# Optimization experiments

Measured on AMD Instinct MI355X. Metric: run time of the kernel, lower is better.

The kernel has to match this reference:

```python
import jax, jax.numpy as jnp
import numpy as np

# ---- constants from OtLlamaAttention __init__ defaults / chosen config ----
Q_LEVELS = 256
Q_LUT_MIN = 0.02004
SMOOTH = 0.9           # stat_smooth_factor (EMA)
Q_SEED = 0
HEAD_DIM = 128
SCALING = HEAD_DIM ** -0.5
N_HEADS, N_KV_HEADS = 32, 8
GROUPS = N_HEADS // N_KV_HEADS  # num_key_value_groups


def _update_qstats(x, old_mm, sf=SMOOTH):
    # q_min_max_quantiles is None -> plain min/max; EMA once stats are finite.
    cur = jax.lax.stop_gradient(jnp.stack([x.min(), x.max()]).astype(old_mm.dtype))
    return jnp.where(jnp.isfinite(old_mm).all(), sf * old_mm + (1.0 - sf) * cur, cur)


def _repeat_kv(x, n_rep):
    # [B, KVH, S, D] -> [B, KVH*n_rep, S, D]
    return jnp.repeat(x, n_rep, axis=1)


def _fq(x, lo, hi, levels=Q_LEVELS):
    # deterministic uniform fake-quant with straight-through estimator
    scale = (hi - lo) / (levels - 1)
    q = jnp.round((jnp.clip(x, lo, hi) - lo) / scale) * scale + lo
    return x + jax.lax.stop_gradient(q - x)


def _fq_b_lut(b, lo, hi, lut_min, levels=Q_LEVELS):
    # weight-side quantization: uniform levels, magnitudes below the modulator
    # LUT minimum (relative to full scale) are not representable -> 0
    scale = (hi - lo) / (levels - 1)
    q = jnp.round((jnp.clip(b, lo, hi) - lo) / scale) * scale + lo
    full_scale = jnp.maximum(jnp.abs(lo), jnp.abs(hi))
    q = jnp.where(jnp.abs(q) < lut_min * full_scale, 0.0, q)
    return b + jax.lax.stop_gradient(q - b)


def _fq_stoch(x, lo, hi, rkey, levels=Q_LEVELS):
    # seeded stochastic rounding on the (optical) accumulator output
    scale = (hi - lo) / (levels - 1)
    t = (jnp.clip(x, lo, hi) - lo) / scale
    u = jax.lax.stop_gradient(jax.random.uniform(rkey, x.shape, dtype=x.dtype))
    q = jnp.floor(t + u) * scale + lo
    return x + jax.lax.stop_gradient(q - x)


def _quantized_matmul(a, b, a_mm, b_mm, o_mm, rkey, skip_quantize=False):
    if skip_quantize:
        return jnp.matmul(a, b)
    aq = _fq(a, a_mm[0], a_mm[1])
    bq = _fq_b_lut(b, b_mm[0], b_mm[1], Q_LUT_MIN)
    out = jnp.matmul(aq, bq)
    return _fq_stoch(out, o_mm[0], o_mm[1], rkey)


def setup_inputs() -> dict:
    key0 = jax.random.key(0)
    k1, k2, k3 = jax.random.split(key0, 3)
    B, S, D = 1, 2048, HEAD_DIM
    query = jax.random.normal(k1, (B, N_HEADS, S, D), dtype=jnp.float32)
    key = jax.random.normal(k2, (B, N_KV_HEADS, S, D), dtype=jnp.float32)
    value = jax.random.normal(k3, (B, N_KV_HEADS, S, D), dtype=jnp.float32)
    causal = jnp.tril(jnp.ones((S, S), dtype=bool))
    attention_mask = jnp.where(causal, 0.0, -1e9).astype(jnp.float32)[None, None]
    inf = jnp.float32(jnp.inf)
    fresh = jnp.array([inf, -inf], dtype=jnp.float32)
    return {
        "query": query, "key": key, "value": value,
        "attention_mask": attention_mask,
        "query_min_max": fresh, "key_min_max": fresh, "qk_min_max": fresh,
        "attn_min_max": jnp.array([0.0, 1.0], dtype=jnp.float32),
        "value_min_max": fresh, "av_min_max": fresh,
    }


def reference(query, key, value, attention_mask, query_min_max, key_min_max,
              qk_min_max, attn_min_max, value_min_max, av_min_max):
    rk = jax.random.key(Q_SEED)
    rk_qk, rk_av = jax.random.split(rk)

    # ---- no_grad stat updates (used immediately, as torch copies in-place) ----
    q_mm = _update_qstats(query, query_min_max)
    k_mm = _update_qstats(key, key_min_max)

    key_states = _repeat_kv(key, GROUPS)      # [B,H,S,D]
    value_states = _repeat_kv(value, GROUPS)

    # qk_min_max starts non-finite -> seeded from an unquantized pass
    raw_qk = jax.lax.stop_gradient(
        jnp.einsum("bhqd,bhkd->bhqk", query, key_states) * SCALING)
    qk_mm = _update_qstats(raw_qk, qk_min_max)

    # ---- quantized QK^T ----
    attn_weights = _quantized_matmul(
        query, jnp.swapaxes(key_states, -1, -2), q_mm, k_mm, qk_mm, rk_qk)
    attn_weights = attn_weights * SCALING
    attn_weights = attn_weights + attention_mask[:, :, :, : key_states.shape[-2]]
    attn_weights = jax.nn.softmax(attn_weights.astype(jnp.float32), axis=-1
                                  ).astype(query.dtype)
    # dropout p=0.0 -> identity

    a_mm = _update_qstats(attn_weights, attn_min_max)
    v_mm = _update_qstats(value_states, value_min_max)
    raw_av = jax.lax.stop_gradient(jnp.matmul(attn_weights, value_states))
    av_mm = _update_qstats(raw_av, av_min_max)

    # ---- quantized AV ----
    attn_output = _quantized_matmul(
        attn_weights, value_states, a_mm, v_mm, av_mm, rk_av,
        skip_quantize=False)

    attn_output = jnp.swapaxes(attn_output, 1, 2)  # [B,S,H,D]
    return attn_output, attn_weights


if __name__ == "__main__":
    out = reference(**setup_inputs())
    print(out[0].shape, out[1].shape)
```

## Files before the change

kernel.cpp:

```cpp
#include <hip/hip_runtime.h>
#include <stdint.h>
#include <math.h>

#pragma clang fp contract(off)

#define NH 32
#define NKVH 8
#define SEQ 2048
#define HD 128
#define SCALING_F 0.08838834764831845f
#define OUT0_N (SEQ*NH*HD)

typedef __attribute__((ext_vector_type(8))) short bf16x8;
typedef __attribute__((ext_vector_type(8))) _Float16 f16x8;
typedef __attribute__((ext_vector_type(8))) unsigned short u16x8;
typedef __attribute__((ext_vector_type(4))) float f32x4;

__host__ __device__ __forceinline__ void tf2x32(uint32_t k0, uint32_t k1,
    uint32_t x0, uint32_t x1, uint32_t* o0, uint32_t* o1) {
  uint32_t k2 = k0 ^ k1 ^ 0x1BD11BDAu;
  x0 += k0; x1 += k1;
#define TFR(r) { x0 += x1; x1 = (x1 << (r)) | (x1 >> (32 - (r))); x1 ^= x0; }
  TFR(13) TFR(15) TFR(26) TFR(6)
  x0 += k1; x1 += k2 + 1u;
  TFR(17) TFR(29) TFR(16) TFR(24)
  x0 += k2; x1 += k0 + 2u;
  TFR(13) TFR(15) TFR(26) TFR(6)
  x0 += k0; x1 += k1 + 3u;
  TFR(17) TFR(29) TFR(16) TFR(24)
  x0 += k1; x1 += k2 + 4u;
  TFR(13) TFR(15) TFR(26) TFR(6)
  x0 += k2; x1 += k0 + 5u;
#undef TFR
  *o0 = x0; *o1 = x1;
}

__device__ __forceinline__ float tf_uniform(uint32_t k0, uint32_t k1, uint32_t idx) {
  uint32_t a, b;
  tf2x32(k0, k1, 0u, idx, &a, &b);
  uint32_t bits = a ^ b;
  return __uint_as_float((bits >> 9) | 0x3f800000u) - 1.0f;
}

__device__ __forceinline__ unsigned fmono(float x) {
  unsigned u = __float_as_uint(x);
  return (u >> 31) ? ~u : (u | 0x80000000u);
}
__device__ __forceinline__ float funmono(unsigned m) {
  return __uint_as_float((m >> 31) ? (m ^ 0x80000000u) : ~m);
}

__device__ __forceinline__ void push_minmax(unsigned* slots, unsigned cm, unsigned cM) {
  volatile unsigned* vs = (volatile unsigned*)slots;
  if (cm < vs[0]) atomicMin(&slots[0], cm);
  if (cM > vs[1]) atomicMax(&slots[1], cM);
}

__device__ __forceinline__ unsigned short f2bf(float x) {
  return (unsigned short)(__float_as_uint(x) >> 16);
}

__device__ __forceinline__ void f16split(float x, unsigned short* h, unsigned short* l) {
  _Float16 hf = (_Float16)x;
  float r = x - (float)hf;
  _Float16 lf = (_Float16)r;
  *h = __builtin_bit_cast(unsigned short, hf);
  *l = __builtin_bit_cast(unsigned short, lf);
}

__device__ __forceinline__ float fq_st_i(float x, float lo, float hi, float scale,
                                         float scinv, float u) {
  float c = fminf(fmaxf(x, lo), hi);
  float t = (c - lo) * scinv;
  return floorf(t + u) * scale + lo;
}

#define SWZ_OFF(row, c16) ((((row) * 256) + ((c16) * 16)) ^ (((row) & 7) << 4))

__device__ __forceinline__ void stage_panel(const unsigned short* __restrict__ g,
                                            int rowstride, unsigned short* s, int tid) {
#pragma unroll
  for (int it = 0; it < 8; ++it) {
    const int i = it * 256 + tid;
    const int row = i >> 4, c16 = i & 15;
    const u16x8 val = *(const u16x8*)&g[(size_t)row * rowstride + c16 * 8];
    *(u16x8*)((char*)s + SWZ_OFF(row, c16)) = val;
  }
}

__device__ __forceinline__ f16x8 frag_h(const unsigned short* s, int row, int c16) {
  return *(const f16x8*)((const char*)s + SWZ_OFF(row, c16));
}
__device__ __forceinline__ bf16x8 frag_b(const unsigned short* s, int row, int c16) {
  return *(const bf16x8*)((const char*)s + SWZ_OFF(row, c16));
}

__global__ void init_ws(unsigned* su) {
  int t = threadIdx.x;
  if (t < 12) su[t] = (t & 1) ? 0u : 0xFFFFFFFFu;
}

__global__ void finalize_kernel(const unsigned* __restrict__ slots,
                                const float* __restrict__ oldmm,
                                float* __restrict__ outc) {
  if (threadIdx.x == 0) {
    float clo = funmono(slots[0]), chi = funmono(slots[1]);
    float o0 = oldmm[0], o1 = oldmm[1];
    bool fin = isfinite(o0) && isfinite(o1);
    float lo = fin ? (0.9f * o0 + 0.1f * clo) : clo;
    float hi = fin ? (0.9f * o1 + 0.1f * chi) : chi;
    float sc = (hi - lo) / 255.0f;
    outc[0] = lo;
    outc[1] = hi;
    outc[2] = sc;
    outc[3] = 0.02004f * fmaxf(fabsf(lo), fabsf(hi));
    outc[4] = 1.0f / sc;
  }
}

__global__ __launch_bounds__(256) void minmax_kernel(const float4* __restrict__ x,
                                                     int n4, unsigned* __restrict__ slots) {
  float lmin = INFINITY, lmax = -INFINITY;
  for (int i = blockIdx.x * blockDim.x + threadIdx.x; i < n4; i += gridDim.x * blockDim.x) {
    float4 a = x[i];
    lmin = fminf(lmin, fminf(fminf(a.x, a.y), fminf(a.z, a.w)));
    lmax = fmaxf(lmax, fmaxf(fmaxf(a.x, a.y), fmaxf(a.z, a.w)));
  }
  __shared__ unsigned bmin, bmax;
  if (threadIdx.x == 0) { bmin = 0xFFFFFFFFu; bmax = 0u; }
  __syncthreads();
  atomicMin(&bmin, fmono(lmin));
  atomicMax(&bmax, fmono(lmax));
  __syncthreads();
  if (threadIdx.x == 0) push_minmax(slots, bmin, bmax);
}

__global__ __launch_bounds__(256) void quant_q_kernel(const float* __restrict__ q,
    unsigned short* __restrict__ qnb, unsigned short* __restrict__ qh,
    unsigned short* __restrict__ ql, const float* __restrict__ cw) {
  const float lo = cw[0], hi = cw[1], sc = cw[2];
  int idx = blockIdx.x * 256 + threadIdx.x;
  float4 x = ((const float4*)q)[idx];
  float xa[4] = {x.x, x.y, x.z, x.w};
  ushort4 o, oh, ol;
  unsigned short* op = (unsigned short*)&o;
  unsigned short* ohp = (unsigned short*)&oh;
  unsigned short* olp = (unsigned short*)&ol;
#pragma unroll
  for (int j = 0; j < 4; ++j) {
    float n = rintf((fminf(fmaxf(xa[j], lo), hi) - lo) / sc);
    op[j] = f2bf(n);
    f16split(xa[j], &ohp[j], &olp[j]);
  }
  ((ushort4*)qnb)[idx] = o;
  ((ushort4*)qh)[idx] = oh;
  ((ushort4*)ql)[idx] = ol;
}

__global__ __launch_bounds__(256) void quant_k_kernel(const float* __restrict__ k,
    unsigned short* __restrict__ kzb, unsigned short* __restrict__ kmb,
    unsigned short* __restrict__ kh, unsigned short* __restrict__ kl,
    float* __restrict__ Zk, float* __restrict__ Mk, const float* __restrict__ cw) {
  const float lo = cw[8], hi = cw[9], sc = cw[10], thr = cw[11];
  const int tid = threadIdx.x;
  const int row = blockIdx.x * 8 + (tid >> 5);
  const int c4 = (tid & 31) * 4;
  float4 x = *(const float4*)&k[(size_t)row * HD + c4];
  float xa[4] = {x.x, x.y, x.z, x.w};
  ushort4 zo, mo, ho, lo_;
  unsigned short* zp = (unsigned short*)&zo;
  unsigned short* mp = (unsigned short*)&mo;
  unsigned short* hp = (unsigned short*)&ho;
  unsigned short* lp = (unsigned short*)&lo_;
  float zs = 0.f, ms = 0.f;
#pragma unroll
  for (int j = 0; j < 4; ++j) {
    float m = rintf((fminf(fmaxf(xa[j], lo), hi) - lo) / sc);
    float kq = m * sc + lo;
    float z = (fabsf(kq) < thr) ? 0.f : 1.f;
    float mq = z * m;
    zs += z; ms += mq;
    zp[j] = f2bf(z); mp[j] = f2bf(mq);
    f16split(xa[j], &hp[j], &lp[j]);
  }
  *(ushort4*)&kzb[(size_t)row * HD + c4] = zo;
  *(ushort4*)&kmb[(size_t)row * HD + c4] = mo;
  *(ushort4*)&kh[(size_t)row * HD + c4] = ho;
  *(ushort4*)&kl[(size_t)row * HD + c4] = lo_;
#pragma unroll
  for (int off = 16; off > 0; off >>= 1) {
    zs += __shfl_xor(zs, off);
    ms += __shfl_xor(ms, off);
  }
  if ((tid & 31) == 0) { Zk[row] = zs; Mk[row] = ms; }
}

__global__ __launch_bounds__(256) void quant_v_kernel(const float* __restrict__ v,
    unsigned short* __restrict__ vzT, unsigned short* __restrict__ vmT,
    unsigned short* __restrict__ vhT, unsigned short* __restrict__ vlT,
    const float* __restrict__ cw) {
  const float lo = cw[16], hi = cw[17], sc = cw[18], thr = cw[19];
  const int kvh = blockIdx.y, dg = blockIdx.x;
  const int tid = threadIdx.x;
  for (int ch = 0; ch < 8; ++ch) {
    int kp = ch * 256 + tid;
    float4 x = *(const float4*)&v[((size_t)(kvh * SEQ + kp)) * HD + dg * 4];
    float xa[4] = {x.x, x.y, x.z, x.w};
#pragma unroll
    for (int j = 0; j < 4; ++j) {
      float m = rintf((fminf(fmaxf(xa[j], lo), hi) - lo) / sc);
      float vq = m * sc + lo;
      float z = (fabsf(vq) < thr) ? 0.f : 1.f;
      float mq = z * m;
      size_t o = ((size_t)(kvh * HD + dg * 4 + j)) * SEQ + kp;
      vzT[o] = f2bf(z);
      vmT[o] = f2bf(mq);
      unsigned short hb, lb;
      f16split(xa[j], &hb, &lb);
      vhT[o] = hb;
      vlT[o] = lb;
    }
  }
}

__global__ __launch_bounds__(256, 2) void qk_raw_mfma(
    const unsigned short* __restrict__ qh, const unsigned short* __restrict__ ql,
    const unsigned short* __restrict__ kh, const unsigned short* __restrict__ kl,
    unsigned* __restrict__ slots) {
  __shared__ __align__(16) unsigned short s_h[128 * 128];
  __shared__ __align__(16) unsigned short s_l[128 * 128];
  const int kbi = blockIdx.x, qbi = blockIdx.y, h = blockIdx.z;
  const int kvh = h >> 2;
  const int tid = threadIdx.x;
  const int wid = tid >> 6, lane = tid & 63;
  const int fr = lane & 15, fg = lane >> 4;
  const int qrow0 = qbi * 128 + wid * 32;
  const int kcol0 = kbi * 128;
  const unsigned short* qhg = qh + (size_t)h * SEQ * HD;
  const unsigned short* qlg = ql + (size_t)h * SEQ * HD;

  stage_panel(kh + ((size_t)kvh * SEQ + kcol0) * HD, HD, s_h, tid);
  stage_panel(kl + ((size_t)kvh * SEQ + kcol0) * HD, HD, s_l, tid);
  __syncthreads();

  f32x4 acc[2][8];
  const f32x4 z4 = {0.f, 0.f, 0.f, 0.f};
#pragma unroll
  for (int rg = 0; rg < 2; ++rg)
#pragma unroll
    for (int cg = 0; cg < 8; ++cg) acc[rg][cg] = z4;

#pragma unroll
  for (int ks = 0; ks < 4; ++ks) {
    const int d0 = ks * 32 + fg * 8;
    const int c16 = ks * 4 + fg;
    const f16x8 a0h = *(const f16x8*)&qhg[(size_t)(qrow0 + fr) * HD + d0];
    const f16x8 a0l = *(const f16x8*)&qlg[(size_t)(qrow0 + fr) * HD + d0];
    const f16x8 a1h = *(const f16x8*)&qhg[(size_t)(qrow0 + 16 + fr) * HD + d0];
    const f16x8 a1l = *(const f16x8*)&qlg[(size_t)(qrow0 + 16 + fr) * HD + d0];
#pragma unroll
    for (int cg = 0; cg < 8; ++cg) {
      const f16x8 bh = frag_h(s_h, cg * 16 + fr, c16);
      const f16x8 bl = frag_h(s_l, cg * 16 + fr, c16);
      acc[0][cg] = __builtin_amdgcn_mfma_f32_16x16x32_f16(a0h, bh, acc[0][cg], 0, 0, 0);
      acc[0][cg] = __builtin_amdgcn_mfma_f32_16x16x32_f16(a0h, bl, acc[0][cg], 0, 0, 0);
      acc[0][cg] = __builtin_amdgcn_mfma_f32_16x16x32_f16(a0l, bh, acc[0][cg], 0, 0, 0);
      acc[1][cg] = __builtin_amdgcn_mfma_f32_16x16x32_f16(a1h, bh, acc[1][cg], 0, 0, 0);
      acc[1][cg] = __builtin_amdgcn_mfma_f32_16x16x32_f16(a1h, bl, acc[1][cg], 0, 0, 0);
      acc[1][cg] = __builtin_amdgcn_mfma_f32_16x16x32_f16(a1l, bh, acc[1][cg], 0, 0, 0);
    }
  }
  float lmin = INFINITY, lmax = -INFINITY;
#pragma unroll
  for (int rg = 0; rg < 2; ++rg)
#pragma unroll
    for (int cg = 0; cg < 8; ++cg)
#pragma unroll
      for (int r = 0; r < 4; ++r) {
        const float rv = acc[rg][cg][r] * SCALING_F;
        lmin = fminf(lmin, rv);
        lmax = fmaxf(lmax, rv);
      }
  __shared__ unsigned bmin, bmax;
  if (tid == 0) { bmin = 0xFFFFFFFFu; bmax = 0u; }
  __syncthreads();
  atomicMin(&bmin, fmono(lmin));
  atomicMax(&bmax, fmono(lmax));
  __syncthreads();
  if (tid == 0) push_minmax(slots, bmin, bmax);
}

__global__ __launch_bounds__(256, 2) void qk_quant_kernel(
    const unsigned short* __restrict__ qnb, const unsigned short* __restrict__ kzb,
    const unsigned short* __restrict__ kmb, const float* __restrict__ Zk,
    const float* __restrict__ Mk, float* __restrict__ qdot,
    const float* __restrict__ cw) {
  const int kbi = blockIdx.x, qbi = blockIdx.y, h = blockIdx.z;
  if (kbi > qbi) return;
  __shared__ __align__(16) unsigned short s_z[128 * 128];
  __shared__ __align__(16) unsigned short s_m[128 * 128];
  const int kvh = h >> 2;
  const float qlo = cw[0], qsc = cw[2];
  const float klo = cw[8], ksc = cw[10];
  const int tid = threadIdx.x;
  const int wid = tid >> 6, lane = tid & 63;
  const int fr = lane & 15, fg = lane >> 4;
  const int qrow0 = qbi * 128 + wid * 32;
  const int kcol0 = kbi * 128;
  const unsigned short* qg = qnb + (size_t)h * SEQ * HD;

  stage_panel(kzb + ((size_t)kvh * SEQ + kcol0) * HD, HD, s_z, tid);
  stage_panel(kmb + ((size_t)kvh * SEQ + kcol0) * HD, HD, s_m, tid);
  __syncthreads();

  f32x4 P[2][8], R[2][8];
  const f32x4 z4 = {0.f, 0.f, 0.f, 0.f};
#pragma unroll
  for (int rg = 0; rg < 2; ++rg)
#pragma unroll
    for (int cg = 0; cg < 8; ++cg) { P[rg][cg] = z4; R[rg][cg] = z4; }

#pragma unroll
  for (int ks = 0; ks < 4; ++ks) {
    const int d0 = ks * 32 + fg * 8;
    const int c16 = ks * 4 + fg;
    const bf16x8 a0 = *(const bf16x8*)&qg[(size_t)(qrow0 + fr) * HD + d0];
    const bf16x8 a1 = *(const bf16x8*)&qg[(size_t)(qrow0 + 16 + fr) * HD + d0];
#pragma unroll
    for (int cg = 0; cg < 8; ++cg) {
      const bf16x8 bz = frag_b(s_z, cg * 16 + fr, c16);
      const bf16x8 bm = frag_b(s_m, cg * 16 + fr, c16);
      P[0][cg] = __builtin_amdgcn_mfma_f32_16x16x32_bf16(a0, bz, P[0][cg], 0, 0, 0);
      P[1][cg] = __builtin_amdgcn_mfma_f32_16x16x32_bf16(a1, bz, P[1][cg], 0, 0, 0);
      R[0][cg] = __builtin_amdgcn_mfma_f32_16x16x32_bf16(a0, bm, R[0][cg], 0, 0, 0);
      R[1][cg] = __builtin_amdgcn_mfma_f32_16x16x32_bf16(a1, bm, R[1][cg], 0, 0, 0);
    }
  }
#pragma unroll
  for (int cg = 0; cg < 8; ++cg) {
    const int col = kcol0 + cg * 16 + fr;
    const float Z = Zk[kvh * SEQ + col], M = Mk[kvh * SEQ + col];
    const float base = qlo * (klo * Z + ksc * M);
#pragma unroll
    for (int rg = 0; rg < 2; ++rg)
#pragma unroll
      for (int r = 0; r < 4; ++r) {
        const int row = qrow0 + rg * 16 + fg * 4 + r;
        qdot[((size_t)h * SEQ + row) * SEQ + col] =
            base + qsc * (klo * P[rg][cg][r] + ksc * R[rg][cg][r]);
      }
  }
}

__global__ __launch_bounds__(256) void softmax_kernel(
    float* __restrict__ attn, const float* __restrict__ cw,
    unsigned* __restrict__ slots, uint32_t uk0, uint32_t uk1) {
  const int row = blockIdx.x;
  const int qi = row & (SEQ - 1);
  const int tid = threadIdx.x;
  const float lo = cw[24], hi = cw[25], sc = cw[26], sci = cw[28];
  float* prow = attn + (size_t)row * SEQ;
  const uint32_t jbase = (uint32_t)row << 11;

  float vals[8];
  float lmax = -INFINITY;
#pragma unroll
  for (int m = 0; m < 2; ++m) {
    int ki = m * 1024 + tid * 4;
    if (ki <= qi) {
      float4 x4 = *(const float4*)&prow[ki];
      float xa[4] = {x4.x, x4.y, x4.z, x4.w};
#pragma unroll
      for (int j = 0; j < 4; ++j) {
        if (ki + j <= qi) {
          float u = tf_uniform(uk0, uk1, jbase + (uint32_t)(ki + j));
          float lg = fq_st_i(xa[j], lo, hi, sc, sci, u) * SCALING_F;
          vals[m * 4 + j] = lg;
          lmax = fmaxf(lmax, lg);
        } else {
          vals[m * 4 + j] = -INFINITY;
        }
      }
    } else {
      vals[m * 4 + 0] = vals[m * 4 + 1] = vals[m * 4 + 2] = vals[m * 4 + 3] = -INFINITY;
    }
  }

  __shared__ float smax[4], ssum[4], smn[4], smx[4];
#pragma unroll
  for (int off = 32; off > 0; off >>= 1) lmax = fmaxf(lmax, __shfl_xor(lmax, off));
  if ((tid & 63) == 0) smax[tid >> 6] = lmax;
  __syncthreads();
  float rmax = fmaxf(fmaxf(smax[0], smax[1]), fmaxf(smax[2], smax[3]));

  float lsum = 0.f;
#pragma unroll
  for (int e = 0; e < 8; ++e) { vals[e] = __expf(vals[e] - rmax); lsum += vals[e]; }
#pragma unroll
  for (int off = 32; off > 0; off >>= 1) lsum += __shfl_xor(lsum, off);
  if ((tid & 63) == 0) ssum[tid >> 6] = lsum;
  __syncthreads();
  float rinv = 1.0f / (ssum[0] + ssum[1] + ssum[2] + ssum[3]);

  float lmin2 = INFINITY, lmax2 = -INFINITY;
#pragma unroll
  for (int m = 0; m < 2; ++m) {
    int ki = m * 1024 + tid * 4;
    float4 st;
    float* stp = (float*)&st;
#pragma unroll
    for (int j = 0; j < 4; ++j) {
      float w = vals[m * 4 + j] * rinv;
      stp[j] = w;
      lmin2 = fminf(lmin2, w);
      lmax2 = fmaxf(lmax2, w);
    }
    *(float4*)&prow[ki] = st;
  }
#pragma unroll
  for (int off = 32; off > 0; off >>= 1) {
    lmin2 = fminf(lmin2, __shfl_xor(lmin2, off));
    lmax2 = fmaxf(lmax2, __shfl_xor(lmax2, off));
  }
  if ((tid & 63) == 0) { smn[tid >> 6] = lmin2; smx[tid >> 6] = lmax2; }
  __syncthreads();
  if (tid == 0) {
    float mn = fminf(fminf(smn[0], smn[1]), fminf(smn[2], smn[3]));
    float mx = fmaxf(fmaxf(smx[0], smx[1]), fmaxf(smx[2], smx[3]));
    push_minmax(slots, fmono(mn), fmono(mx));
  }
}

__device__ __forceinline__ void pack_split8(const float* __restrict__ p,
                                            f16x8* ah, f16x8* al) {
  float4 w0 = *(const float4*)p;
  float4 w1 = *(const float4*)(p + 4);
  float wa[8] = {w0.x, w0.y, w0.z, w0.w, w1.x, w1.y, w1.z, w1.w};
  f16x8 h, l;
#pragma unroll
  for (int j = 0; j < 8; ++j) {
    _Float16 hf = (_Float16)wa[j];
    h[j] = hf;
    l[j] = (_Float16)(wa[j] - (float)hf);
  }
  *ah = h; *al = l;
}

__global__ __launch_bounds__(256, 2) void av_raw_mfma(
    const float* __restrict__ attn, const unsigned short* __restrict__ vhT,
    const unsigned short* __restrict__ vlT, unsigned* __restrict__ slots) {
  __shared__ __align__(16) unsigned short s_h[128 * 128];
  __shared__ __align__(16) unsigned short s_l[128 * 128];
  const int qbi = (int)gridDim.x - 1 - (int)blockIdx.x;
  const int h = blockIdx.y, kvh = h >> 2;
  const int tid = threadIdx.x;
  const int wid = tid >> 6, lane = tid & 63;
  const int fr = lane & 15, fg = lane >> 4;
  const int qrow0 = qbi * 128 + wid * 32;
  const float* ag = attn + (size_t)h * SEQ * SEQ;
  const unsigned short* bhg = vhT + (size_t)kvh * HD * SEQ;
  const unsigned short* blg = vlT + (size_t)kvh * HD * SEQ;
  const int nc = qbi + 1;
  f32x4 acc[2][8];
  const f32x4 z4 = {0.f, 0.f, 0.f, 0.f};
#pragma unroll
  for (int rg = 0; rg < 2; ++rg)
#pragma unroll
    for (int cg = 0; cg < 8; ++cg) acc[rg][cg] = z4;

  for (int c = 0; c < nc; ++c) {
    __syncthreads();
    stage_panel(bhg + c * 128, SEQ, s_h, tid);
    stage_panel(blg + c * 128, SEQ, s_l, tid);
    __syncthreads();
#pragma unroll
    for (int ks = 0; ks < 4; ++ks) {
      const int kp0 = c * 128 + ks * 32 + fg * 8;
      const int c16 = ks * 4 + fg;
      f16x8 a0h, a0l, a1h, a1l;
      pack_split8(ag + (size_t)(qrow0 + fr) * SEQ + kp0, &a0h, &a0l);
      pack_split8(ag + (size_t)(qrow0 + 16 + fr) * SEQ + kp0, &a1h, &a1l);
#pragma unroll
      for (int cg = 0; cg < 8; ++cg) {
        const f16x8 bh = frag_h(s_h, cg * 16 + fr, c16);
        const f16x8 bl = frag_h(s_l, cg * 16 + fr, c16);
        acc[0][cg] = __builtin_amdgcn_mfma_f32_16x16x32_f16(a0h, bh, acc[0][cg], 0, 0, 0);
        acc[0][cg] = __builtin_amdgcn_mfma_f32_16x16x32_f16(a0h, bl, acc[0][cg], 0, 0, 0);
        acc[0][cg] = __builtin_amdgcn_mfma_f32_16x16x32_f16(a0l, bh, acc[0][cg], 0, 0, 0);
        acc[1][cg] = __builtin_amdgcn_mfma_f32_16x16x32_f16(a1h, bh, acc[1][cg], 0, 0, 0);
        acc[1][cg] = __builtin_amdgcn_mfma_f32_16x16x32_f16(a1h, bl, acc[1][cg], 0, 0, 0);
        acc[1][cg] = __builtin_amdgcn_mfma_f32_16x16x32_f16(a1l, bh, acc[1][cg], 0, 0, 0);
      }
    }
  }
  float lmin = INFINITY, lmax = -INFINITY;
#pragma unroll
  for (int rg = 0; rg < 2; ++rg)
#pragma unroll
    for (int cg = 0; cg < 8; ++cg)
#pragma unroll
      for (int r = 0; r < 4; ++r) {
        lmin = fminf(lmin, acc[rg][cg][r]);
        lmax = fmaxf(lmax, acc[rg][cg][r]);
      }
  __shared__ unsigned bmin, bmax;
  if (tid == 0) { bmin = 0xFFFFFFFFu; bmax = 0u; }
  __syncthreads();
  atomicMin(&bmin, fmono(lmin));
  atomicMax(&bmax, fmono(lmax));
  __syncthreads();
  if (tid == 0) push_minmax(slots, bmin, bmax);
}

__device__ __forceinline__ bf16x8 pack_a8(const float* __restrict__ ar,
                                          float lo, float hi, float sc) {
  float4 w0 = *(const float4*)ar;
  float4 w1 = *(const float4*)(ar + 4);
  float wa[8] = {w0.x, w0.y, w0.z, w0.w, w1.x, w1.y, w1.z, w1.w};
  bf16x8 r;
#pragma unroll
  for (int j = 0; j < 8; ++j) {
    float n = rintf((fminf(fmaxf(wa[j], lo), hi) - lo) / sc);
    r[j] = (short)(__float_as_uint(n) >> 16);
  }
  return r;
}

__global__ __launch_bounds__(256, 2) void av_quant_kernel(
    const float* __restrict__ attn, const unsigned short* __restrict__ vzT,
    const unsigned short* __restrict__ vmT, float* __restrict__ out0,
    const float* __restrict__ cw) {
  __shared__ __align__(16) unsigned short s_z[128 * 128];
  __shared__ __align__(16) unsigned short s_m[128 * 128];
  const int qbi = (int)gridDim.x - 1 - (int)blockIdx.x;
  const int h = blockIdx.y, kvh = h >> 2;
  const float alo = cw[32], ahi = cw[33], asc = cw[34];
  const float vlo = cw[16], vsc = cw[18];
  const int tid = threadIdx.x;
  const int wid = tid >> 6, lane = tid & 63;
  const int fr = lane & 15, fg = lane >> 4;
  const int qrow0 = qbi * 128 + wid * 32;
  const float* ag = attn + (size_t)h * SEQ * SEQ;
  const unsigned short* zg = vzT + (size_t)kvh * HD * SEQ;
  const unsigned short* mg = vmT + (size_t)kvh * HD * SEQ;
  const int nc = qbi + 1;
  f32x4 P[2][8], R[2][8];
  const f32x4 z4 = {0.f, 0.f, 0.f, 0.f};
#pragma unroll
  for (int rg = 0; rg < 2; ++rg)
#pragma unroll
    for (int cg = 0; cg < 8; ++cg) { P[rg][cg] = z4; R[rg][cg] = z4; }

  for (int c = 0; c < nc; ++c) {
    __syncthreads();
    stage_panel(zg + c * 128, SEQ, s_z, tid);
    stage_panel(mg + c * 128, SEQ, s_m, tid);
    __syncthreads();
#pragma unroll
    for (int ks = 0; ks < 4; ++ks) {
      const int kp0 = c * 128 + ks * 32 + fg * 8;
      const int c16 = ks * 4 + fg;
      const bf16x8 a0 = pack_a8(ag + (size_t)(qrow0 + fr) * SEQ + kp0, alo, ahi, asc);
      const bf16x8 a1 = pack_a8(ag + (size_t)(qrow0 + 16 + fr) * SEQ + kp0, alo, ahi, asc);
#pragma unroll
      for (int cg = 0; cg < 8; ++cg) {
        const bf16x8 bz = frag_b(s_z, cg * 16 + fr, c16);
        const bf16x8 bm = frag_b(s_m, cg * 16 + fr, c16);
        P[0][cg] = __builtin_amdgcn_mfma_f32_16x16x32_bf16(a0, bz, P[0][cg], 0, 0, 0);
        P[1][cg] = __builtin_amdgcn_mfma_f32_16x16x32_bf16(a1, bz, P[1][cg], 0, 0, 0);
        R[0][cg] = __builtin_amdgcn_mfma_f32_16x16x32_bf16(a0, bm, R[0][cg], 0, 0, 0);
        R[1][cg] = __builtin_amdgcn_mfma_f32_16x16x32_bf16(a1, bm, R[1][cg], 0, 0, 0);
      }
    }
  }
#pragma unroll
  for (int cg = 0; cg < 8; ++cg) {
    const int dcol = cg * 16 + fr;
#pragma unroll
    for (int rg = 0; rg < 2; ++rg)
#pragma unroll
      for (int r = 0; r < 4; ++r) {
        const int row = qrow0 + rg * 16 + fg * 4 + r;
        out0[((size_t)row * NH + h) * HD + dcol] =
            asc * (vlo * P[rg][cg][r] + vsc * R[rg][cg][r]);
      }
  }
}

__global__ __launch_bounds__(256) void stoch_kernel(float* __restrict__ out0,
                                                    const float* __restrict__ cw,
                                                    uint32_t uk0, uint32_t uk1) {
  int idx = blockIdx.x * 256 + threadIdx.x;
  const float lo = cw[40], hi = cw[41], sc = cw[42], sci = cw[44];
  int qi = idx >> 12;
  int rem = idx & 4095;
  int h = rem >> 7, d = rem & 127;
  uint32_t j = ((uint32_t)h * SEQ + (uint32_t)qi) * HD + (uint32_t)d;
  float x = out0[idx];
  float u = tf_uniform(uk0, uk1, j);
  out0[idx] = fq_st_i(x, lo, hi, sc, sci, u);
}

extern "C" void kernel_launch(void* const* d_in, const int* in_sizes, int n_in,
                              void* d_out, int out_size, void* d_ws, size_t ws_size,
                              hipStream_t stream) {
  (void)in_sizes; (void)n_in; (void)out_size; (void)ws_size;
  const float* q      = (const float*)d_in[0];
  const float* k      = (const float*)d_in[1];
  const float* v      = (const float*)d_in[2];
  const float* q_old  = (const float*)d_in[4];
  const float* k_old  = (const float*)d_in[5];
  const float* qk_old = (const float*)d_in[6];
  const float* a_old  = (const float*)d_in[7];
  const float* v_old  = (const float*)d_in[8];
  const float* av_old = (const float*)d_in[9];
  float* out0 = (float*)d_out;
  float* out1 = out0 + (size_t)OUT0_N;
  unsigned* su = (unsigned*)d_ws;
  float* cw = (float*)d_ws + 16;

  unsigned short* vzT = (unsigned short*)((char*)d_ws + 1024);
  unsigned short* vmT = vzT + (size_t)NKVH * SEQ * HD;
  float* Zk = (float*)(vmT + (size_t)NKVH * SEQ * HD);
  float* Mk = Zk + NKVH * SEQ;

  unsigned short* qnb = (unsigned short*)out0;
  unsigned short* kzb = qnb + (size_t)NH * SEQ * HD;
  unsigned short* kmb = kzb + (size_t)NKVH * SEQ * HD;
  unsigned short* vhT = kmb + (size_t)NKVH * SEQ * HD;
  unsigned short* vlT = vhT + (size_t)NKVH * SEQ * HD;

  unsigned short* qh = (unsigned short*)out1;
  unsigned short* ql = qh + (size_t)NH * SEQ * HD;
  unsigned short* kh = ql + (size_t)NH * SEQ * HD;
  unsigned short* kl = kh + (size_t)NKVH * SEQ * HD;

  uint32_t kq0, kq1, ka0, ka1;
  tf2x32(0u, 0u, 0u, 0u, &kq0, &kq1);
  tf2x32(0u, 0u, 0u, 1u, &ka0, &ka1);

  init_ws<<<1, 32, 0, stream>>>(su);
  minmax_kernel<<<1024, 256, 0, stream>>>((const float4*)q, (NH * SEQ * HD) / 4, su + 0);
  minmax_kernel<<<512, 256, 0, stream>>>((const float4*)k, (NKVH * SEQ * HD) / 4, su + 2);
  minmax_kernel<<<512, 256, 0, stream>>>((const float4*)v, (NKVH * SEQ * HD) / 4, su + 4);
  finalize_kernel<<<1, 1, 0, stream>>>(su + 0, q_old, cw + 0);
  finalize_kernel<<<1, 1, 0, stream>>>(su + 2, k_old, cw + 8);
  finalize_kernel<<<1, 1, 0, stream>>>(su + 4, v_old, cw + 16);

  quant_q_kernel<<<(NH * SEQ * HD) / 4 / 256, 256, 0, stream>>>(q, qnb, qh, ql, cw);
  quant_k_kernel<<<(NKVH * SEQ) / 8, 256, 0, stream>>>(k, kzb, kmb, kh, kl, Zk, Mk, cw);
  quant_v_kernel<<<dim3(32, NKVH), 256, 0, stream>>>(v, vzT, vmT, vhT, vlT, cw);

  qk_raw_mfma<<<dim3(16, 16, NH), 256, 0, stream>>>(qh, ql, kh, kl, su + 6);
  finalize_kernel<<<1, 1, 0, stream>>>(su + 6, qk_old, cw + 24);
  qk_quant_kernel<<<dim3(16, 16, NH), 256, 0, stream>>>(qnb, kzb, kmb, Zk, Mk, out1, cw);

  softmax_kernel<<<NH * SEQ, 256, 0, stream>>>(out1, cw, su + 8, kq0, kq1);
  finalize_kernel<<<1, 1, 0, stream>>>(su + 8, a_old, cw + 32);

  av_raw_mfma<<<dim3(16, NH), 256, 0, stream>>>(out1, vhT, vlT, su + 10);
  finalize_kernel<<<1, 1, 0, stream>>>(su + 10, av_old, cw + 40);
  av_quant_kernel<<<dim3(16, NH), 256, 0, stream>>>(out1, vzT, vmT, out0, cw);

  stoch_kernel<<<OUT0_N / 256, 256, 0, stream>>>(out0, cw, ka0, ka1);
}
```

Baseline: 1.566 ms.

## Fuse raw and quantized AV matmuls; merge minmax, finalize and prep launches

Replaces the separate raw-AV and quantized-AV passes with one fused kernel that reads each attention tile once, packs it into quantized bf16 and f16 hi/lo forms, and runs all MFMA chains together over 64-row query tiles with 64-wide K panels. Moving the V hi/lo buffers into the workspace frees out0 so the fused kernel can write it directly; the fused path runs only when the workspace is at least 18 MB. It also merges the three minmax launches, the three finalize launches and the three quant launches into single kernels to cut launch overhead. The fused kernel keeps more accumulators live (three sets of eight), which raises register pressure, and it uses smaller panels.

```diff
diff --git a/kernel.cpp b/kernel.cpp
--- a/kernel.cpp
+++ b/kernel.cpp
@@ -76,6 +76,7 @@
 }
 
 #define SWZ_OFF(row, c16) ((((row) * 256) + ((c16) * 16)) ^ (((row) & 7) << 4))
+#define SWZ64_OFF(row, c16) ((((row) * 128) + ((c16) * 16)) ^ (((row) & 7) << 4))
 
 __device__ __forceinline__ void stage_panel(const unsigned short* __restrict__ g,
                                             int rowstride, unsigned short* s, int tid) {
@@ -88,11 +89,28 @@
   }
 }
 
+__device__ __forceinline__ void stage_panel64(const unsigned short* __restrict__ g,
+                                              int rowstride, unsigned short* s, int tid) {
+#pragma unroll
+  for (int it = 0; it < 4; ++it) {
+    const int i = it * 256 + tid;
+    const int row = i >> 3, c16 = i & 7;
+    const u16x8 val = *(const u16x8*)&g[(size_t)row * rowstride + c16 * 8];
+    *(u16x8*)((char*)s + SWZ64_OFF(row, c16)) = val;
+  }
+}
+
 __device__ __forceinline__ f16x8 frag_h(const unsigned short* s, int row, int c16) {
   return *(const f16x8*)((const char*)s + SWZ_OFF(row, c16));
 }
 __device__ __forceinline__ bf16x8 frag_b(const unsigned short* s, int row, int c16) {
   return *(const bf16x8*)((const char*)s + SWZ_OFF(row, c16));
+}
+__device__ __forceinline__ f16x8 frag_h64(const unsigned short* s, int row, int c16) {
+  return *(const f16x8*)((const char*)s + SWZ64_OFF(row, c16));
+}
+__device__ __forceinline__ bf16x8 frag_b64(const unsigned short* s, int row, int c16) {
+  return *(const bf16x8*)((const char*)s + SWZ64_OFF(row, c16));
 }
 
 __global__ void init_ws(unsigned* su) {
@@ -100,28 +118,50 @@
   if (t < 12) su[t] = (t & 1) ? 0u : 0xFFFFFFFFu;
 }
 
+__device__ __forceinline__ void finalize_one(const unsigned* slots,
+                                             const float* oldmm, float* outc) {
+  float clo = funmono(slots[0]), chi = funmono(slots[1]);
+  float o0 = oldmm[0], o1 = oldmm[1];
+  bool fin = isfinite(o0) && isfinite(o1);
+  float lo = fin ? (0.9f * o0 + 0.1f * clo) : clo;
+  float hi = fin ? (0.9f * o1 + 0.1f * chi) : chi;
+  float sc = (hi - lo) / 255.0f;
+  outc[0] = lo;
+  outc[1] = hi;
+  outc[2] = sc;
+  outc[3] = 0.02004f * fmaxf(fabsf(lo), fabsf(hi));
+  outc[4] = 1.0f / sc;
+}
+
 __global__ void finalize_kernel(const unsigned* __restrict__ slots,
                                 const float* __restrict__ oldmm,
                                 float* __restrict__ outc) {
-  if (threadIdx.x == 0) {
-    float clo = funmono(slots[0]), chi = funmono(slots[1]);
-    float o0 = oldmm[0], o1 = oldmm[1];
-    bool fin = isfinite(o0) && isfinite(o1);
-    float lo = fin ? (0.9f * o0 + 0.1f * clo) : clo;
-    float hi = fin ? (0.9f * o1 + 0.1f * chi) : chi;
-    float sc = (hi - lo) / 255.0f;
-    outc[0] = lo;
-    outc[1] = hi;
-    outc[2] = sc;
-    outc[3] = 0.02004f * fmaxf(fabsf(lo), fabsf(hi));
-    outc[4] = 1.0f / sc;
-  }
-}
-
-__global__ __launch_bounds__(256) void minmax_kernel(const float4* __restrict__ x,
-                                                     int n4, unsigned* __restrict__ slots) {
+  if (threadIdx.x == 0) finalize_one(slots, oldmm, outc);
+}
+
+__global__ void finalize3_kernel(const unsigned* __restrict__ su,
+                                 const float* __restrict__ q_old,
+                                 const float* __restrict__ k_old,
+                                 const float* __restrict__ v_old,
+                                 float* __restrict__ cw) {
+  int t = threadIdx.x;
+  if (t == 0) finalize_one(su + 0, q_old, cw + 0);
+  else if (t == 1) finalize_one(su + 2, k_old, cw + 8);
+  else if (t == 2) finalize_one(su + 4, v_old, cw + 16);
+}
+
+__global__ __launch_bounds__(256) void minmax3_kernel(const float4* __restrict__ q,
+    const float4* __restrict__ k, const float4* __restrict__ v,
+    unsigned* __restrict__ su) {
+  const int b = blockIdx.x;
+  const float4* x;
+  int n4, b0, nb;
+  unsigned* slots;
+  if (b < 1024) { x = q; n4 = (NH * SEQ * HD) / 4; b0 = 0; nb = 1024; slots = su + 0; }
+  else if (b < 1536) { x = k; n4 = (NKVH * SEQ * HD) / 4; b0 = 1024; nb = 512; slots = su + 2; }
+  else { x = v; n4 = (NKVH * SEQ * HD) / 4; b0 = 1536; nb = 512; slots = su + 4; }
   float lmin = INFINITY, lmax = -INFINITY;
-  for (int i = blockIdx.x * blockDim.x + threadIdx.x; i < n4; i += gridDim.x * blockDim.x) {
+  for (int i = (b - b0) * 256 + threadIdx.x; i < n4; i += nb * 256) {
     float4 a = x[i];
     lmin = fminf(lmin, fminf(fminf(a.x, a.y), fminf(a.z, a.w)));
     lmax = fmaxf(lmax, fmaxf(fmaxf(a.x, a.y), fmaxf(a.z, a.w)));
@@ -135,90 +175,92 @@
   if (threadIdx.x == 0) push_minmax(slots, bmin, bmax);
 }
 
-__global__ __launch_bounds__(256) void quant_q_kernel(const float* __restrict__ q,
+#define PREP_QB 8192
+#define PREP_KB 2048
+#define PREP_VB 256
+__global__ __launch_bounds__(256) void prep_kernel(const float* __restrict__ q,
+    const float* __restrict__ k, const float* __restrict__ v,
     unsigned short* __restrict__ qnb, unsigned short* __restrict__ qh,
-    unsigned short* __restrict__ ql, const float* __restrict__ cw) {
-  const float lo = cw[0], hi = cw[1], sc = cw[2];
-  int idx = blockIdx.x * 256 + threadIdx.x;
-  float4 x = ((const float4*)q)[idx];
-  float xa[4] = {x.x, x.y, x.z, x.w};
-  ushort4 o, oh, ol;
-  unsigned short* op = (unsigned short*)&o;
-  unsigned short* ohp = (unsigned short*)&oh;
-  unsigned short* olp = (unsigned short*)&ol;
-#pragma unroll
-  for (int j = 0; j < 4; ++j) {
-    float n = rintf((fminf(fmaxf(xa[j], lo), hi) - lo) / sc);
-    op[j] = f2bf(n);
-    f16split(xa[j], &ohp[j], &olp[j]);
-  }
-  ((ushort4*)qnb)[idx] = o;
-  ((ushort4*)qh)[idx] = oh;
-  ((ushort4*)ql)[idx] = ol;
-}
-
-__global__ __launch_bounds__(256) void quant_k_kernel(const float* __restrict__ k,
+    unsigned short* __restrict__ ql,
     unsigned short* __restrict__ kzb, unsigned short* __restrict__ kmb,
     unsigned short* __restrict__ kh, unsigned short* __restrict__ kl,
-    float* __restrict__ Zk, float* __restrict__ Mk, const float* __restrict__ cw) {
-  const float lo = cw[8], hi = cw[9], sc = cw[10], thr = cw[11];
-  const int tid = threadIdx.x;
-  const int row = blockIdx.x * 8 + (tid >> 5);
-  const int c4 = (tid & 31) * 4;
-  float4 x = *(const float4*)&k[(size_t)row * HD + c4];
-  float xa[4] = {x.x, x.y, x.z, x.w};
-  ushort4 zo, mo, ho, lo_;
-  unsigned short* zp = (unsigned short*)&zo;
-  unsigned short* mp = (unsigned short*)&mo;
-  unsigned short* hp = (unsigned short*)&ho;
-  unsigned short* lp = (unsigned short*)&lo_;
-  float zs = 0.f, ms = 0.f;
-#pragma unroll
-  for (int j = 0; j < 4; ++j) {
-    float m = rintf((fminf(fmaxf(xa[j], lo), hi) - lo) / sc);
-    float kq = m * sc + lo;
-    float z = (fabsf(kq) < thr) ? 0.f : 1.f;
-    float mq = z * m;
-    zs += z; ms += mq;
-    zp[j] = f2bf(z); mp[j] = f2bf(mq);
-    f16split(xa[j], &hp[j], &lp[j]);
-  }
-  *(ushort4*)&kzb[(size_t)row * HD + c4] = zo;
-  *(ushort4*)&kmb[(size_t)row * HD + c4] = mo;
-  *(ushort4*)&kh[(size_t)row * HD + c4] = ho;
-  *(ushort4*)&kl[(size_t)row * HD + c4] = lo_;
-#pragma unroll
-  for (int off = 16; off > 0; off >>= 1) {
-    zs += __shfl_xor(zs, off);
-    ms += __shfl_xor(ms, off);
-  }
-  if ((tid & 31) == 0) { Zk[row] = zs; Mk[row] = ms; }
-}
-
-__global__ __launch_bounds__(256) void quant_v_kernel(const float* __restrict__ v,
+    float* __restrict__ Zk, float* __restrict__ Mk,
     unsigned short* __restrict__ vzT, unsigned short* __restrict__ vmT,
     unsigned short* __restrict__ vhT, unsigned short* __restrict__ vlT,
     const float* __restrict__ cw) {
-  const float lo = cw[16], hi = cw[17], sc = cw[18], thr = cw[19];
-  const int kvh = blockIdx.y, dg = blockIdx.x;
-  const int tid = threadIdx.x;
-  for (int ch = 0; ch < 8; ++ch) {
-    int kp = ch * 256 + tid;
-    float4 x = *(const float4*)&v[((size_t)(kvh * SEQ + kp)) * HD + dg * 4];
+  const int b = blockIdx.x, tid = threadIdx.x;
+  if (b < PREP_QB) {
+    const float lo = cw[0], hi = cw[1], sc = cw[2];
+    int idx = b * 256 + tid;
+    float4 x = ((const float4*)q)[idx];
     float xa[4] = {x.x, x.y, x.z, x.w};
+    ushort4 o, oh, ol;
+    unsigned short* op = (unsigned short*)&o;
+    unsigned short* ohp = (unsigned short*)&oh;
+    unsigned short* olp = (unsigned short*)&ol;
+#pragma unroll
+    for (int j = 0; j < 4; ++j) {
+      float n = rintf((fminf(fmaxf(xa[j], lo), hi) - lo) / sc);
+      op[j] = f2bf(n);
+      f16split(xa[j], &ohp[j], &olp[j]);
+    }
+    ((ushort4*)qnb)[idx] = o;
+    ((ushort4*)qh)[idx] = oh;
+    ((ushort4*)ql)[idx] = ol;
+  } else if (b < PREP_QB + PREP_KB) {
+    const float lo = cw[8], hi = cw[9], sc = cw[10], thr = cw[11];
+    const int row = (b - PREP_QB) * 8 + (tid >> 5);
+    const int c4 = (tid & 31) * 4;
+    float4 x = *(const float4*)&k[(size_t)row * HD + c4];
+    float xa[4] = {x.x, x.y, x.z, x.w};
+    ushort4 zo, mo, ho, lo_;
+    unsigned short* zp = (unsigned short*)&zo;
+    unsigned short* mp = (unsigned short*)&mo;
+    unsigned short* hp = (unsigned short*)&ho;
+    unsigned short* lp = (unsigned short*)&lo_;
+    float zs = 0.f, ms = 0.f;
 #pragma unroll
     for (int j = 0; j < 4; ++j) {
       float m = rintf((fminf(fmaxf(xa[j], lo), hi) - lo) / sc);
-      float vq = m * sc + lo;
-      float z = (fabsf(vq) < thr) ? 0.f : 1.f;
+      float kq = m * sc + lo;
+      float z = (fabsf(kq) < thr) ? 0.f : 1.f;
       float mq = z * m;
-      size_t o = ((size_t)(kvh * HD + dg * 4 + j)) * SEQ + kp;
-      vzT[o] = f2bf(z);
-      vmT[o] = f2bf(mq);
-      unsigned short hb, lb;
-      f16split(xa[j], &hb, &lb);
-      vhT[o] = hb;
-      vlT[o] = lb;
+      zs += z; ms += mq;
+      zp[j] = f2bf(z); mp[j] = f2bf(mq);
+      f16split(xa[j], &hp[j], &lp[j]);
+    }
+    *(ushort4*)&kzb[(size_t)row * HD + c4] = zo;
+    *(ushort4*)&kmb[(size_t)row * HD + c4] = mo;
+    *(ushort4*)&kh[(size_t)row * HD + c4] = ho;
+    *(ushort4*)&kl[(size_t)row * HD + c4] = lo_;
+#pragma unroll
+    for (int off = 16; off > 0; off >>= 1) {
+      zs += __shfl_xor(zs, off);
+      ms += __shfl_xor(ms, off);
+    }
+    if ((tid & 31) == 0) { Zk[row] = zs; Mk[row] = ms; }
+  } else {
+    const float lo = cw[16], hi = cw[17], sc = cw[18], thr = cw[19];
+    const int b2 = b - (PREP_QB + PREP_KB);
+    const int kvh = b2 >> 5, dg = b2 & 31;
+    for (int ch = 0; ch < 8; ++ch) {
+      int kp = ch * 256 + tid;
+      float4 x = *(const float4*)&v[((size_t)(kvh * SEQ + kp)) * HD + dg * 4];
+      float xa[4] = {x.x, x.y, x.z, x.w};
+#pragma unroll
+      for (int j = 0; j < 4; ++j) {
+        float m = rintf((fminf(fmaxf(xa[j], lo), hi) - lo) / sc);
+        float vq = m * sc + lo;
+        float z = (fabsf(vq) < thr) ? 0.f : 1.f;
+        float mq = z * m;
+        size_t o = ((size_t)(kvh * HD + dg * 4 + j)) * SEQ + kp;
+        vzT[o] = f2bf(z);
+        vmT[o] = f2bf(mq);
+        unsigned short hb, lb;
+        f16split(xa[j], &hb, &lb);
+        vhT[o] = hb;
+        vlT[o] = lb;
+      }
     }
   }
 }
@@ -446,6 +488,37 @@
   *ah = h; *al = l;
 }
 
+__device__ __forceinline__ bf16x8 pack_a8(const float* __restrict__ ar,
+                                          float lo, float hi, float sc) {
+  float4 w0 = *(const float4*)ar;
+  float4 w1 = *(const float4*)(ar + 4);
+  float wa[8] = {w0.x, w0.y, w0.z, w0.w, w1.x, w1.y, w1.z, w1.w};
+  bf16x8 r;
+#pragma unroll
+  for (int j = 0; j < 8; ++j) {
+    float n = rintf((fminf(fmaxf(wa[j], lo), hi) - lo) / sc);
+    r[j] = (short)(__float_as_uint(n) >> 16);
+  }
+  return r;
+}
+
+__device__ __forceinline__ void pack_all(const float* __restrict__ p,
+    float lo, float hi, float sc, bf16x8* an, f16x8* ah, f16x8* al) {
+  float4 w0 = *(const float4*)p;
+  float4 w1 = *(const float4*)(p + 4);
+  float wa[8] = {w0.x, w0.y, w0.z, w0.w, w1.x, w1.y, w1.z, w1.w};
+  bf16x8 n8; f16x8 h8, l8;
+#pragma unroll
+  for (int j = 0; j < 8; ++j) {
+    float n = rintf((fminf(fmaxf(wa[j], lo), hi) - lo) / sc);
+    n8[j] = (short)(__float_as_uint(n) >> 16);
+    _Float16 hf = (_Float16)wa[j];
+    h8[j] = hf;
+    l8[j] = (_Float16)(wa[j] - (float)hf);
+  }
+  *an = n8; *ah = h8; *al = l8;
+}
+
 __global__ __launch_bounds__(256, 2) void av_raw_mfma(
     const float* __restrict__ attn, const unsigned short* __restrict__ vhT,
     const unsigned short* __restrict__ vlT, unsigned* __restrict__ slots) {
@@ -510,20 +583,6 @@
   atomicMax(&bmax, fmono(lmax));
   __syncthreads();
   if (tid == 0) push_minmax(slots, bmin, bmax);
-}
-
-__device__ __forceinline__ bf16x8 pack_a8(const float* __restrict__ ar,
-                                          float lo, float hi, float sc) {
-  float4 w0 = *(const float4*)ar;
-  float4 w1 = *(const float4*)(ar + 4);
-  float wa[8] = {w0.x, w0.y, w0.z, w0.w, w1.x, w1.y, w1.z, w1.w};
-  bf16x8 r;
-#pragma unroll
-  for (int j = 0; j < 8; ++j) {
-    float n = rintf((fminf(fmaxf(wa[j], lo), hi) - lo) / sc);
-    r[j] = (short)(__float_as_uint(n) >> 16);
-  }
-  return r;
 }
 
 __global__ __launch_bounds__(256, 2) void av_quant_kernel(
@@ -587,6 +646,90 @@
   }
 }
 
+__global__ __launch_bounds__(256, 2) void av_fused_kernel(
+    const float* __restrict__ attn,
+    const unsigned short* __restrict__ vzT, const unsigned short* __restrict__ vmT,
+    const unsigned short* __restrict__ vhT, const unsigned short* __restrict__ vlT,
+    float* __restrict__ out0, const float* __restrict__ cw,
+    unsigned* __restrict__ slots) {
+  __shared__ __align__(16) unsigned short s_z[128 * 64];
+  __shared__ __align__(16) unsigned short s_m[128 * 64];
+  __shared__ __align__(16) unsigned short s_h[128 * 64];
+  __shared__ __align__(16) unsigned short s_l[128 * 64];
+  const int qbi2 = (int)gridDim.x - 1 - (int)blockIdx.x;
+  const int h = blockIdx.y, kvh = h >> 2;
+  const float alo = cw[32], ahi = cw[33], asc = cw[34];
+  const float vlo = cw[16], vsc = cw[18];
+  const int tid = threadIdx.x;
+  const int wid = tid >> 6, lane = tid & 63;
+  const int fr = lane & 15, fg = lane >> 4;
+  const int qrow0 = qbi2 * 64 + wid * 16;
+  const float* ag = attn + (size_t)h * SEQ * SEQ;
+  const unsigned short* zg = vzT + (size_t)kvh * HD * SEQ;
+  const unsigned short* mg = vmT + (size_t)kvh * HD * SEQ;
+  const unsigned short* hg = vhT + (size_t)kvh * HD * SEQ;
+  const unsigned short* lg = vlT + (size_t)kvh * HD * SEQ;
+  const int nc = qbi2 + 1;
+  f32x4 A[8], P[8], R[8];
+  const f32x4 z4 = {0.f, 0.f, 0.f, 0.f};
+#pragma unroll
+  for (int cg = 0; cg < 8; ++cg) { A[cg] = z4; P[cg] = z4; R[cg] = z4; }
+
+  for (int c = 0; c < nc; ++c) {
+    __syncthreads();
+    stage_panel64(zg + c * 64, SEQ, s_z, tid);
+    stage_panel64(mg + c * 64, SEQ, s_m, tid);
+    stage_panel64(hg + c * 64, SEQ, s_h, tid);
+    stage_panel64(lg + c * 64, SEQ, s_l, tid);
+    __syncthreads();
+#pragma unroll
+    for (int ks = 0; ks < 2; ++ks) {
+      const int kp0 = c * 64 + ks * 32 + fg * 8;
+      const int c16 = ks * 4 + fg;
+      bf16x8 an; f16x8 ah, al;
+      pack_all(ag + (size_t)(qrow0 + fr) * SEQ + kp0, alo, ahi, asc, &an, &ah, &al);
+#pragma unroll
+      for (int cg = 0; cg < 8; ++cg) {
+        const int brow = cg * 16 + fr;
+        const bf16x8 bz = frag_b64(s_z, brow, c16);
+        const bf16x8 bm = frag_b64(s_m, brow, c16);
+        const f16x8 bh = frag_h64(s_h, brow, c16);
+        const f16x8 bl = frag_h64(s_l, brow, c16);
+        P[cg] = __builtin_amdgcn_mfma_f32_16x16x32_bf16(an, bz, P[cg], 0, 0, 0);
+        R[cg] = __builtin_amdgcn_mfma_f32_16x16x32_bf16(an, bm, R[cg], 0, 0, 0);
+        A[cg] = __builtin_amdgcn_mfma_f32_16x16x32_f16(ah, bh, A[cg], 0, 0, 0);
+        A[cg] = __builtin_amdgcn_mfma_f32_16x16x32_f16(ah, bl, A[cg], 0, 0, 0);
+        A[cg] = __builtin_amdgcn_mfma_f32_16x16x32_f16(al, bh, A[cg], 0, 0, 0);
+      }
+    }
+  }
+  float lmin = INFINITY, lmax = -INFINITY;
+#pragma unroll
+  for (int cg = 0; cg < 8; ++cg)
+#pragma unroll
+    for (int r = 0; r < 4; ++r) {
+      lmin = fminf(lmin, A[cg][r]);
+      lmax = fmaxf(lmax, A[cg][r]);
+    }
+#pragma unroll
+  for (int cg = 0; cg < 8; ++cg) {
+    const int dcol = cg * 16 + fr;
+#pragma unroll
+    for (int r = 0; r < 4; ++r) {
+      const int row = qrow0 + fg * 4 + r;
+      out0[((size_t)row * NH + h) * HD + dcol] =
+          asc * (vlo * P[cg][r] + vsc * R[cg][r]);
+    }
+  }
+  __shared__ unsigned bmin, bmax;
+  if (tid == 0) { bmin = 0xFFFFFFFFu; bmax = 0u; }
+  __syncthreads();
+  atomicMin(&bmin, fmono(lmin));
+  atomicMax(&bmax, fmono(lmax));
+  __syncthreads();
+  if (tid == 0) push_minmax(slots, bmin, bmax);
+}
+
 __global__ __launch_bounds__(256) void stoch_kernel(float* __restrict__ out0,
                                                     const float* __restrict__ cw,
                                                     uint32_t uk0, uint32_t uk1) {
@@ -604,7 +747,7 @@
 extern "C" void kernel_launch(void* const* d_in, const int* in_sizes, int n_in,
                               void* d_out, int out_size, void* d_ws, size_t ws_size,
                               hipStream_t stream) {
-  (void)in_sizes; (void)n_in; (void)out_size; (void)ws_size;
+  (void)in_sizes; (void)n_in; (void)out_size;
   const float* q      = (const float*)d_in[0];
   const float* k      = (const float*)d_in[1];
   const float* v      = (const float*)d_in[2];
@@ -623,12 +766,17 @@
   unsigned short* vmT = vzT + (size_t)NKVH * SEQ * HD;
   float* Zk = (float*)(vmT + (size_t)NKVH * SEQ * HD);
   float* Mk = Zk + NKVH * SEQ;
+  unsigned short* vhT_ws = (unsigned short*)(Mk + NKVH * SEQ);
+  unsigned short* vlT_ws = vhT_ws + (size_t)NKVH * SEQ * HD;
+  const int use_fused = ws_size >= (size_t)18 * 1024 * 1024;
 
   unsigned short* qnb = (unsigned short*)out0;
   unsigned short* kzb = qnb + (size_t)NH * SEQ * HD;
   unsigned short* kmb = kzb + (size_t)NKVH * SEQ * HD;
-  unsigned short* vhT = kmb + (size_t)NKVH * SEQ * HD;
-  unsigned short* vlT = vhT + (size_t)NKVH * SEQ * HD;
+  unsigned short* vhT_o = kmb + (size_t)NKVH * SEQ * HD;
+  unsigned short* vlT_o = vhT_o + (size_t)NKVH * SEQ * HD;
+  unsigned short* vhT = use_fused ? vhT_ws : vhT_o;
+  unsigned short* vlT = use_fused ? vlT_ws : vlT_o;
 
   unsigned short* qh = (unsigned short*)out1;
   unsigned short* ql = qh + (size_t)NH * SEQ * HD;
@@ -640,16 +788,11 @@
   tf2x32(0u, 0u, 0u, 1u, &ka0, &ka1);
 
   init_ws<<<1, 32, 0, stream>>>(su);
-  minmax_kernel<<<1024, 256, 0, stream>>>((const float4*)q, (NH * SEQ * HD) / 4, su + 0);
-  minmax_kernel<<<512, 256, 0, stream>>>((const float4*)k, (NKVH * SEQ * HD) / 4, su + 2);
-  minmax_kernel<<<512, 256, 0, stream>>>((const float4*)v, (NKVH * SEQ * HD) / 4, su + 4);
-  finalize_kernel<<<1, 1, 0, stream>>>(su + 0, q_old, cw + 0);
-  finalize_kernel<<<1, 1, 0, stream>>>(su + 2, k_old, cw + 8);
-  finalize_kernel<<<1, 1, 0, stream>>>(su + 4, v_old, cw + 16);
-
-  quant_q_kernel<<<(NH * SEQ * HD) / 4 / 256, 256, 0, stream>>>(q, qnb, qh, ql, cw);
-  quant_k_kernel<<<(NKVH * SEQ) / 8, 256, 0, stream>>>(k, kzb, kmb, kh, kl, Zk, Mk, cw);
-  quant_v_kernel<<<dim3(32, NKVH), 256, 0, stream>>>(v, vzT, vmT, vhT, vlT, cw);
+  minmax3_kernel<<<2048, 256, 0, stream>>>((const float4*)q, (const float4*)k,
+                                           (const float4*)v, su);
+  finalize3_kernel<<<1, 32, 0, stream>>>(su, q_old, k_old, v_old, cw);
+  prep_kernel<<<PREP_QB + PREP_KB + PREP_VB, 256, 0, stream>>>(
+      q, k, v, qnb, qh, ql, kzb, kmb, kh, kl, Zk, Mk, vzT, vmT, vhT, vlT, cw);
 
   qk_raw_mfma<<<dim3(16, 16, NH), 256, 0, stream>>>(qh, ql, kh, kl, su + 6);
   finalize_kernel<<<1, 1, 0, stream>>>(su + 6, qk_old, cw + 24);
@@ -658,9 +801,15 @@
   softmax_kernel<<<NH * SEQ, 256, 0, stream>>>(out1, cw, su + 8, kq0, kq1);
   finalize_kernel<<<1, 1, 0, stream>>>(su + 8, a_old, cw + 32);
 
-  av_raw_mfma<<<dim3(16, NH), 256, 0, stream>>>(out1, vhT, vlT, su + 10);
-  finalize_kernel<<<1, 1, 0, stream>>>(su + 10, av_old, cw + 40);
-  av_quant_kernel<<<dim3(16, NH), 256, 0, stream>>>(out1, vzT, vmT, out0, cw);
+  if (use_fused) {
+    av_fused_kernel<<<dim3(32, NH), 256, 0, stream>>>(out1, vzT, vmT, vhT, vlT,
+                                                      out0, cw, su + 10);
+    finalize_kernel<<<1, 1, 0, stream>>>(su + 10, av_old, cw + 40);
+  } else {
+    av_raw_mfma<<<dim3(16, NH), 256, 0, stream>>>(out1, vhT, vlT, su + 10);
+    finalize_kernel<<<1, 1, 0, stream>>>(su + 10, av_old, cw + 40);
+    av_quant_kernel<<<dim3(16, NH), 256, 0, stream>>>(out1, vzT, vmT, out0, cw);
+  }
 
   stoch_kernel<<<OUT0_N / 256, 256, 0, stream>>>(out0, cw, ka0, ka1);
 }
```

New measurement: 1.758 ms. 12.2% more time.
